# Performance work log

Measured on AMD Instinct MI355X. Metric: run time of the kernel, lower is better.

Reference implementation:

```python
import jax, jax.numpy as jnp
import numpy as np

P_X = 2  # pooling window height
P_Y = 2  # pooling window width
SAMPLE_KEY = 42  # fixed key for the multinomial draw (torch uses global RNG)


def setup_inputs() -> dict:
    key = jax.random.key(0)
    k1, k2, k3 = jax.random.split(key, 3)
    P = P_X * P_Y
    c = jax.random.normal(k1, (16, 64, 256, 256), dtype=jnp.float32)
    # nn.Linear default init ~ U(-1/sqrt(fan_in), 1/sqrt(fan_in)); fan_in = P
    bound = 1.0 / np.sqrt(P)
    W1 = jax.random.uniform(k2, (P, P), jnp.float32, -bound, bound)
    W2 = jax.random.uniform(k3, (P, P), jnp.float32, -bound, bound)
    return {"c": c, "W1": W1, "W2": W2}


def reference(c, W1, W2):
    B, C, H, W = c.shape
    n, m = H // P_X, W // P_Y
    P = P_X * P_Y
    # [B,C,H,W] -> non-overlapping tiles [B,C,n,m,P], flattened row-major per tile
    tiles = c.reshape(B, C, n, P_X, m, P_Y).transpose(0, 1, 2, 4, 3, 5).reshape(B, C, n, m, P)
    # pooling_layer: Linear -> tanh -> Linear -> softmax (all over last dim, size P)
    h = jnp.tanh(jnp.einsum("bcnmp,qp->bcnmq", tiles, W1))
    logits = jnp.einsum("bcnmp,qp->bcnmq", h, W2)
    eta = jax.nn.softmax(logits, axis=-1)  # [B,C,n,m,P]
    # multinomial(eta, 1) == categorical sampling with logits (softmax-invariant)
    zeta = jax.random.categorical(jax.random.key(SAMPLE_KEY), logits, axis=-1)  # [B,C,n,m]
    pooled = jnp.take_along_axis(tiles, zeta[..., None], axis=-1)[..., 0]  # [B,C,n,m]
    return pooled, eta
```

## Files before the change

kernel.cpp:

```cpp
#include <hip/hip_runtime.h>
#include <math.h>


#define NTILES 16777216u
#define NBLOCKS 65536u

__device__ __forceinline__ unsigned rotl32(unsigned x, int r) {
  return (x << r) | (x >> (32 - r));
}

__device__ __forceinline__ unsigned tf_bits(unsigned i) {
  const unsigned k0 = 0u;
  const unsigned k1 = 42u;
  const unsigned k2 = 0x1BD11BDAu ^ 0u ^ 42u;
  unsigned x0 = 0u + k0;
  unsigned x1 = i + k1;
#define TF_ROUND(r) { x0 += x1; x1 = rotl32(x1, (r)); x1 ^= x0; }
  TF_ROUND(13) TF_ROUND(15) TF_ROUND(26) TF_ROUND(6)
  x0 += k1; x1 += k2 + 1u;
  TF_ROUND(17) TF_ROUND(29) TF_ROUND(16) TF_ROUND(24)
  x0 += k2; x1 += k0 + 2u;
  TF_ROUND(13) TF_ROUND(15) TF_ROUND(26) TF_ROUND(6)
  x0 += k0; x1 += k1 + 3u;
  TF_ROUND(17) TF_ROUND(29) TF_ROUND(16) TF_ROUND(24)
  x0 += k1; x1 += k2 + 4u;
  TF_ROUND(13) TF_ROUND(15) TF_ROUND(26) TF_ROUND(6)
  x0 += k2; x1 += k0 + 5u;
#undef TF_ROUND
  return x0 ^ x1;
}

__device__ __forceinline__ float xla_logf(float a) {
  unsigned b = __float_as_uint(a);
  int e = (int)(b >> 23) - 126;
  float m = __uint_as_float((b & 0x007fffffu) | 0x3f000000u);
  bool small = m < 0.70710678118654752440f;
  e -= small ? 1 : 0;
  float m1 = m - 1.0f;
  m = small ? (m1 + m) : m1;
  float z = m * m;
  float y = 7.0376836292e-2f;
  y = fmaf(y, m, -1.1514610310e-1f);
  y = fmaf(y, m,  1.1676998740e-1f);
  y = fmaf(y, m, -1.2420140846e-1f);
  y = fmaf(y, m,  1.4249322787e-1f);
  y = fmaf(y, m, -1.6668057665e-1f);
  y = fmaf(y, m,  2.0000714765e-1f);
  y = fmaf(y, m, -2.4999993993e-1f);
  y = fmaf(y, m,  3.3333331174e-1f);
  y = y * m;
  y = y * z;
  float ef = (float)e;
  y = fmaf(ef, -2.12194440e-4f, y);
  y = fmaf(-0.5f, z, y);
  float r = m + y;
  r = fmaf(ef, 0.693359375f, r);
  return r;
}

__device__ __forceinline__ float xla_tanhf(float x) {
  float ax = fabsf(x);
  float xc = fminf(fmaxf(x, -7.99881172180175781f), 7.99881172180175781f);
  float x2 = xc * xc;
  float num = -2.76076847742355e-16f;
  num = fmaf(x2, num,  2.00018790482477e-13f);
  num = fmaf(x2, num, -8.60467152213735e-11f);
  num = fmaf(x2, num,  5.12229709037114e-08f);
  num = fmaf(x2, num,  1.48572235717979e-05f);
  num = fmaf(x2, num,  6.37261928875436e-04f);
  num = fmaf(x2, num,  4.89352455891786e-03f);
  num = xc * num;
  float den = 1.19825839466702e-06f;
  den = fmaf(x2, den, 1.18534705686654e-04f);
  den = fmaf(x2, den, 2.26843463243900e-03f);
  den = fmaf(x2, den, 4.89352518554385e-03f);
  float r = num / den;
  return (ax < 0.0004f) ? x : r;
}

__global__ __launch_bounds__(256) void pool_sample_kernel(
    const float* __restrict__ c,
    const float* __restrict__ w1,
    const float* __restrict__ w2,
    float* __restrict__ pooled,
    float* __restrict__ eta) {
  unsigned t = blockIdx.x * 256u + threadIdx.x;
  unsigned j  = t & 127u;
  unsigned i  = (t >> 7) & 127u;
  unsigned bc = t >> 14;

  size_t off = ((size_t)bc * 256u + 2u * i) * 256u + 2u * j;
  float2 r0 = *reinterpret_cast<const float2*>(c + off);
  float2 r1 = *reinterpret_cast<const float2*>(c + off + 256u);
  float t0 = r0.x, t1 = r0.y, t2 = r1.x, t3 = r1.y;

  float a1[16], a2[16];
#pragma unroll
  for (int k = 0; k < 16; ++k) { a1[k] = w1[k]; a2[k] = w2[k]; }

  float h[4];
#pragma unroll
  for (int q = 0; q < 4; ++q) {
    float acc = a1[q * 4 + 0] * t0;
    acc = fmaf(a1[q * 4 + 1], t1, acc);
    acc = fmaf(a1[q * 4 + 2], t2, acc);
    acc = fmaf(a1[q * 4 + 3], t3, acc);
    h[q] = xla_tanhf(acc);
  }

  float l[4];
#pragma unroll
  for (int q = 0; q < 4; ++q) {
    float acc = a2[q * 4 + 0] * h[0];
    acc = fmaf(a2[q * 4 + 1], h[1], acc);
    acc = fmaf(a2[q * 4 + 2], h[2], acc);
    acc = fmaf(a2[q * 4 + 3], h[3], acc);
    l[q] = acc;
  }

  float mx = fmaxf(fmaxf(l[0], l[1]), fmaxf(l[2], l[3]));
  float e0 = expf(l[0] - mx);
  float e1 = expf(l[1] - mx);
  float e2 = expf(l[2] - mx);
  float e3 = expf(l[3] - mx);
  float inv = 1.0f / (((e0 + e1) + e2) + e3);

  unsigned base = 4u * t;
  float best = 0.0f;
  int z = 0;
#pragma unroll
  for (int q = 0; q < 4; ++q) {
    unsigned bits = tf_bits(base + (unsigned)q);
    float f = __uint_as_float((bits >> 9) | 0x3f800000u) - 1.0f;
    float u = (f == 0.0f) ? 1.17549435e-38f : f;
    float tl = xla_logf(u);
    float g = -xla_logf(-tl);
    float lq = (q == 0) ? l[0] : (q == 1) ? l[1] : (q == 2) ? l[2] : l[3];
    float v = g + lq;
    if (q == 0) { best = v; z = 0; }
    else if (v > best) { best = v; z = q; }
  }

  float pv = t0;
  if (z == 1) pv = t1;
  if (z == 2) pv = t2;
  if (z == 3) pv = t3;

  pooled[t] = pv;
  *reinterpret_cast<float4*>(eta + (size_t)base) =
      make_float4(e0 * inv, e1 * inv, e2 * inv, e3 * inv);
}

extern "C" void kernel_launch(void* const* d_in, const int* in_sizes, int n_in,
                              void* d_out, int out_size, void* d_ws, size_t ws_size,
                              hipStream_t stream) {
  const float* c  = (const float*)d_in[0];
  const float* w1 = (const float*)d_in[1];
  const float* w2 = (const float*)d_in[2];
  float* pooled = (float*)d_out;
  float* eta    = (float*)d_out + (size_t)NTILES;

  pool_sample_kernel<<<dim3(NBLOCKS), dim3(256), 0, stream>>>(c, w1, w2, pooled, eta);
}
```

Measured before the change: 642.5 us.

## Use fast hardware log/exp with exact fallback near ties, two tiles per thread

Each thread now handles two adjacent 2x2 tiles using float4 loads. The Gumbel noise is computed with the hardware log2 instruction, and the exact XLA-style log path is rerun only when the top two perturbed logits fall within a small margin. The softmax drops the max subtraction and uses hardware exp2 and reciprocal. This removes ALU work, but skipping max subtraction risks overflow for large logits and the fast path could still differ from the exact argmax.

```diff
diff --git a/kernel.cpp b/kernel.cpp
--- a/kernel.cpp
+++ b/kernel.cpp
@@ -2,8 +2,8 @@
 #include <math.h>
 
 
-#define NTILES 16777216u
-#define NBLOCKS 65536u
+#define NTILES   16777216u
+#define NBLOCKS  32768u
 
 __device__ __forceinline__ unsigned rotl32(unsigned x, int r) {
   return (x << r) | (x >> (32 - r));
@@ -78,26 +78,23 @@
   return (ax < 0.0004f) ? x : r;
 }
 
-__global__ __launch_bounds__(256) void pool_sample_kernel(
-    const float* __restrict__ c,
-    const float* __restrict__ w1,
-    const float* __restrict__ w2,
-    float* __restrict__ pooled,
-    float* __restrict__ eta) {
-  unsigned t = blockIdx.x * 256u + threadIdx.x;
-  unsigned j  = t & 127u;
-  unsigned i  = (t >> 7) & 127u;
-  unsigned bc = t >> 14;
+__device__ __forceinline__ float exact_gumbel(float u) {
+  float tl = xla_logf(u);
+  return -xla_logf(-tl);
+}
 
-  size_t off = ((size_t)bc * 256u + 2u * i) * 256u + 2u * j;
-  float2 r0 = *reinterpret_cast<const float2*>(c + off);
-  float2 r1 = *reinterpret_cast<const float2*>(c + off + 256u);
-  float t0 = r0.x, t1 = r0.y, t2 = r1.x, t3 = r1.y;
+__device__ __forceinline__ float fast_gumbel(float u) {
+  float lg = __builtin_amdgcn_logf(u);
+  float tn = lg * -0.69314718f;
+  return __builtin_amdgcn_logf(tn) * -0.69314718f;
+}
 
-  float a1[16], a2[16];
-#pragma unroll
-  for (int k = 0; k < 16; ++k) { a1[k] = w1[k]; a2[k] = w2[k]; }
+#define MARGIN_EPS 2.0e-4f
 
+__device__ __forceinline__ void process_tile(
+    unsigned t, float t0, float t1, float t2, float t3,
+    const float* __restrict__ a1, const float* __restrict__ a2,
+    float* __restrict__ pooled, float* __restrict__ eta) {
   float h[4];
 #pragma unroll
   for (int q = 0; q < 4; ++q) {
@@ -107,7 +104,6 @@
     acc = fmaf(a1[q * 4 + 3], t3, acc);
     h[q] = xla_tanhf(acc);
   }
-
   float l[4];
 #pragma unroll
   for (int q = 0; q < 4; ++q) {
@@ -118,27 +114,39 @@
     l[q] = acc;
   }
 
-  float mx = fmaxf(fmaxf(l[0], l[1]), fmaxf(l[2], l[3]));
-  float e0 = expf(l[0] - mx);
-  float e1 = expf(l[1] - mx);
-  float e2 = expf(l[2] - mx);
-  float e3 = expf(l[3] - mx);
-  float inv = 1.0f / (((e0 + e1) + e2) + e3);
+  float e0 = __builtin_amdgcn_exp2f(l[0] * 1.442695041f);
+  float e1 = __builtin_amdgcn_exp2f(l[1] * 1.442695041f);
+  float e2 = __builtin_amdgcn_exp2f(l[2] * 1.442695041f);
+  float e3 = __builtin_amdgcn_exp2f(l[3] * 1.442695041f);
+  float inv = __builtin_amdgcn_rcpf(((e0 + e1) + e2) + e3);
 
   unsigned base = 4u * t;
-  float best = 0.0f;
-  int z = 0;
+  float u[4];
 #pragma unroll
   for (int q = 0; q < 4; ++q) {
     unsigned bits = tf_bits(base + (unsigned)q);
     float f = __uint_as_float((bits >> 9) | 0x3f800000u) - 1.0f;
-    float u = (f == 0.0f) ? 1.17549435e-38f : f;
-    float tl = xla_logf(u);
-    float g = -xla_logf(-tl);
-    float lq = (q == 0) ? l[0] : (q == 1) ? l[1] : (q == 2) ? l[2] : l[3];
-    float v = g + lq;
-    if (q == 0) { best = v; z = 0; }
-    else if (v > best) { best = v; z = q; }
+    u[q] = (f == 0.0f) ? 1.17549435e-38f : f;
+  }
+
+  float best = fast_gumbel(u[0]) + l[0];
+  float second = -3.402823466e+38f;
+  int z = 0;
+#pragma unroll
+  for (int q = 1; q < 4; ++q) {
+    float v = fast_gumbel(u[q]) + l[q];
+    if (v > best) { second = best; best = v; z = q; }
+    else if (v > second) { second = v; }
+  }
+
+  if (best - second < MARGIN_EPS) {
+    float vb = exact_gumbel(u[0]) + l[0];
+    z = 0;
+#pragma unroll
+    for (int q = 1; q < 4; ++q) {
+      float v = exact_gumbel(u[q]) + l[q];
+      if (v > vb) { vb = v; z = q; }
+    }
   }
 
   float pv = t0;
@@ -149,6 +157,30 @@
   pooled[t] = pv;
   *reinterpret_cast<float4*>(eta + (size_t)base) =
       make_float4(e0 * inv, e1 * inv, e2 * inv, e3 * inv);
+}
+
+__global__ __launch_bounds__(256) void pool_sample_kernel(
+    const float* __restrict__ c,
+    const float* __restrict__ w1,
+    const float* __restrict__ w2,
+    float* __restrict__ pooled,
+    float* __restrict__ eta) {
+  unsigned u = blockIdx.x * 256u + threadIdx.x;
+  unsigned jj = u & 63u;
+  unsigned i  = (u >> 6) & 127u;
+  unsigned bc = u >> 13;
+
+  float a1[16], a2[16];
+#pragma unroll
+  for (int k = 0; k < 16; ++k) { a1[k] = w1[k]; a2[k] = w2[k]; }
+
+  size_t off = ((size_t)bc * 256u + 2u * i) * 256u + 4u * jj;
+  float4 rA = *reinterpret_cast<const float4*>(c + off);
+  float4 rB = *reinterpret_cast<const float4*>(c + off + 256u);
+
+  unsigned t0 = (bc << 14) | (i << 7) | (jj << 1);
+  process_tile(t0,     rA.x, rA.y, rB.x, rB.y, a1, a2, pooled, eta);
+  process_tile(t0 + 1, rA.z, rA.w, rB.z, rB.w, a1, a2, pooled, eta);
 }
 
 extern "C" void kernel_launch(void* const* d_in, const int* in_sizes, int n_in,
```

Result: faster. 540.6 us (-15.9%).
